# Kernel optimization log

Measured on AMD Instinct MI355X. Metric: run time of the kernel, lower is better.

Reference implementation:

```python
import jax, jax.numpy as jnp
import numpy as np

S, B, D_DEC, D_ALIGN, D_ENC = 1024, 64, 1024, 1024, 1024


def setup_inputs() -> dict:
    key = jax.random.key(0)
    ks = jax.random.split(key, 6)
    scale = 1.0 / np.sqrt(D_DEC)
    return {
        "s_tm1": jax.random.normal(ks[0], (B, D_DEC), jnp.float32),
        "xs_h": jax.random.normal(ks[1], (S, B, D_ENC), jnp.float32),
        "uh": jax.random.normal(ks[2], (S, B, D_ALIGN), jnp.float32),
        "xs_mask": jnp.ones((S, B), jnp.float32),
        "sa_w": jax.random.normal(ks[3], (D_ALIGN, D_DEC), jnp.float32) * scale,
        "sa_b": jnp.zeros((D_ALIGN,), jnp.float32),
        "a1_w": jax.random.normal(ks[4], (1, D_ALIGN), jnp.float32) * scale,
        "a1_b": jnp.zeros((1,), jnp.float32),
    }


def reference(s_tm1, xs_h, uh, xs_mask, sa_w, sa_b, a1_w, a1_b):
    # sa(s_tm1): [B, align]
    sa_s = s_tm1 @ sa_w.T + sa_b
    # broadcast-add over seq dim, tanh, then a1 (align -> 1), squeeze -> [S, B]
    h = jnp.tanh(sa_s[None, :, :] + uh)                  # [S, B, align]
    e = jnp.einsum('sba,a->sb', h, a1_w[0]) + a1_b[0]    # [S, B]
    # masked softmax over dim 0 (seq)
    ex = jnp.exp(e - jnp.max(e, axis=0, keepdims=True))
    ex = ex * xs_mask
    e_ij = ex / jnp.sum(ex, axis=0, keepdims=True)       # [S, B]
    # weighted sum over seq: [B, D_enc]
    attend = jnp.einsum('sb,sbd->bd', e_ij, xs_h)
    return (e_ij, attend)
```

## Files before the change

kernel.cpp:

```cpp
#include <hip/hip_runtime.h>
#include <hip/hip_bf16.h>

#define S_DIM 1024
#define B_DIM 64
#define A_DIM 1024

#define K2_CONST 2.8853900817779268f

#define K_TILE 64
#define KSPLIT 16
#define A_TILE 64
#define SSPLIT 16
#define S_CHUNK 64

__device__ __forceinline__ float fast_exp2(float x) { return __builtin_amdgcn_exp2f(x); }
__device__ __forceinline__ float fast_rcp(float x)  { return __builtin_amdgcn_rcpf(x); }

__global__ __launch_bounds__(256) void gemm_partial_kernel(
    const float* __restrict__ s_tm1,
    const float* __restrict__ sa_w,
    float* __restrict__ part)
{
    __shared__ float sW[K_TILE][68];
    __shared__ float sS[K_TILE][68];
    const int a0 = blockIdx.x * A_TILE;
    const int k0 = blockIdx.y * K_TILE;
    const int t  = threadIdx.x;

    #pragma unroll
    for (int i = 0; i < 4; ++i) {
        int idx = t + 256 * i;
        int row = idx >> 4;
        int c4  = (idx & 15) * 4;
        float4 v = *(const float4*)(sa_w + (size_t)(a0 + row) * 1024 + k0 + c4);
        sW[c4 + 0][row] = v.x; sW[c4 + 1][row] = v.y;
        sW[c4 + 2][row] = v.z; sW[c4 + 3][row] = v.w;
        float4 u = *(const float4*)(s_tm1 + (size_t)row * 1024 + k0 + c4);
        sS[c4 + 0][row] = u.x; sS[c4 + 1][row] = u.y;
        sS[c4 + 2][row] = u.z; sS[c4 + 3][row] = u.w;
    }
    __syncthreads();

    const int ta = (t & 15) * 4;
    const int tb = (t >> 4) * 4;
    float acc[4][4] = {};
    #pragma unroll 8
    for (int k = 0; k < K_TILE; ++k) {
        float4 wa = *(const float4*)&sW[k][ta];
        float4 sb = *(const float4*)&sS[k][tb];
        float wv[4] = {wa.x, wa.y, wa.z, wa.w};
        float sv[4] = {sb.x, sb.y, sb.z, sb.w};
        #pragma unroll
        for (int i = 0; i < 4; ++i)
            #pragma unroll
            for (int j = 0; j < 4; ++j)
                acc[i][j] = fmaf(wv[i], sv[j], acc[i][j]);
    }

    float* outp = part + (size_t)blockIdx.y * (B_DIM * 1024);
    #pragma unroll
    for (int j = 0; j < 4; ++j) {
        float4 v = {acc[0][j], acc[1][j], acc[2][j], acc[3][j]};
        *(float4*)(outp + (size_t)(tb + j) * 1024 + a0 + ta) = v;
    }
}

__global__ __launch_bounds__(256) void gemm_reduce_kernel(
    const float* __restrict__ part, const float* __restrict__ sa_b,
    float* __restrict__ ksa)
{
    int idx = blockIdx.x * 256 + threadIdx.x;
    int a = idx & 1023;
    float s = sa_b[a];
    #pragma unroll
    for (int kz = 0; kz < KSPLIT; ++kz)
        s += part[(size_t)kz * 65536 + idx];
    ksa[idx] = K2_CONST * s;
}

__global__ __launch_bounds__(256) void fused_kernel(
    const float* __restrict__ uh,
    const float* __restrict__ xs_h,
    const float* __restrict__ ksa,
    const float* __restrict__ a1_w,
    const float* __restrict__ xs_mask,
    float* __restrict__ ex_buf,
    float* __restrict__ psum,
    float* __restrict__ part)
{
    const int b    = blockIdx.x;
    const int sz   = blockIdx.y;
    const int s0   = sz * S_CHUNK;
    const int t    = threadIdx.x;
    const int lane = t & 63;
    const int w    = t >> 6;

    __shared__ float s_ex[S_CHUNK];

    const float4* sap = (const float4*)(ksa + (size_t)b * 1024);
    const float4* awp = (const float4*)a1_w;
    float4 sv[4], aw[4];
    #pragma unroll
    for (int j = 0; j < 4; ++j) { sv[j] = sap[lane + 64 * j]; aw[j] = awp[lane + 64 * j]; }

    for (int k = 0; k < 16; ++k) {
        const int i = w + 4 * k;
        const int s = s0 + i;
        const float4* uhp = (const float4*)(uh + ((size_t)s * B_DIM + b) * 1024);
        float mrow = xs_mask[(size_t)s * B_DIM + b];
        float acc = 0.f;
        #pragma unroll
        for (int j = 0; j < 4; ++j) {
            float4 u = uhp[lane + 64 * j];
            float t0 = fast_exp2(fmaf(K2_CONST, u.x, sv[j].x));
            float t1 = fast_exp2(fmaf(K2_CONST, u.y, sv[j].y));
            float t2 = fast_exp2(fmaf(K2_CONST, u.z, sv[j].z));
            float t3 = fast_exp2(fmaf(K2_CONST, u.w, sv[j].w));
            acc = fmaf(aw[j].x, fast_rcp(1.0f + t0), acc);
            acc = fmaf(aw[j].y, fast_rcp(1.0f + t1), acc);
            acc = fmaf(aw[j].z, fast_rcp(1.0f + t2), acc);
            acc = fmaf(aw[j].w, fast_rcp(1.0f + t3), acc);
        }
        #pragma unroll
        for (int off = 32; off; off >>= 1) acc += __shfl_xor(acc, off);
        if (lane == 0) s_ex[i] = fast_exp2(-K2_CONST * acc) * mrow;
    }
    __syncthreads();

    float4 acc4 = {0.f, 0.f, 0.f, 0.f};
    #pragma unroll 8
    for (int i = 0; i < S_CHUNK; ++i) {
        float wgt = s_ex[i];
        float4 x = *(const float4*)(xs_h + (((size_t)(s0 + i) * B_DIM + b) * 1024) + t * 4);
        acc4.x = fmaf(wgt, x.x, acc4.x); acc4.y = fmaf(wgt, x.y, acc4.y);
        acc4.z = fmaf(wgt, x.z, acc4.z); acc4.w = fmaf(wgt, x.w, acc4.w);
    }
    ((float4*)part)[((size_t)sz * B_DIM + b) * 256 + t] = acc4;

    if (t < S_CHUNK)
        ex_buf[(size_t)(s0 + t) * B_DIM + b] = s_ex[t];

    if (w == 0) {
        float v = s_ex[lane];
        #pragma unroll
        for (int off = 32; off; off >>= 1) v += __shfl_xor(v, off);
        if (lane == 0) psum[sz * B_DIM + b] = v;
    }
}

__global__ __launch_bounds__(256) void finalize_kernel(
    const float* __restrict__ ex_buf, const float* __restrict__ part,
    const float* __restrict__ psum,
    float* __restrict__ eij_out, float* __restrict__ att_out)
{
    const int blk = blockIdx.x;
    const int t = threadIdx.x;
    if (blk < 256) {
        int idx = blk * 256 + t;
        int b = idx & 63;
        float ssum = 0.f;
        #pragma unroll
        for (int sz = 0; sz < SSPLIT; ++sz) ssum += psum[sz * B_DIM + b];
        eij_out[idx] = ex_buf[idx] * (1.0f / ssum);
    } else {
        int idx = (blk - 256) * 256 + t;
        int b = idx >> 10;
        float ssum = 0.f;
        #pragma unroll
        for (int sz = 0; sz < SSPLIT; ++sz) ssum += psum[sz * B_DIM + b];
        float acc = 0.f;
        #pragma unroll
        for (int sz = 0; sz < SSPLIT; ++sz) acc += part[(size_t)sz * 65536 + idx];
        att_out[idx] = acc * (1.0f / ssum);
    }
}

extern "C" void kernel_launch(void* const* d_in, const int* in_sizes, int n_in,
                              void* d_out, int out_size, void* d_ws, size_t ws_size,
                              hipStream_t stream) {
    const float* s_tm1   = (const float*)d_in[0];
    const float* xs_h    = (const float*)d_in[1];
    const float* uh      = (const float*)d_in[2];
    const float* xs_mask = (const float*)d_in[3];
    const float* sa_w    = (const float*)d_in[4];
    const float* sa_b    = (const float*)d_in[5];
    const float* a1_w    = (const float*)d_in[6];

    float* eij_out = (float*)d_out;
    float* att_out = (float*)d_out + S_DIM * B_DIM;

    float* part_gemm = (float*)d_ws;
    float* ksa       = part_gemm + (size_t)KSPLIT * B_DIM * 1024;
    float* ex_buf    = ksa + 65536;
    float* part_att  = ex_buf + 65536;
    float* psum      = part_att + (size_t)SSPLIT * B_DIM * 1024;

    gemm_partial_kernel<<<dim3(A_DIM / A_TILE, KSPLIT), 256, 0, stream>>>(s_tm1, sa_w, part_gemm);
    gemm_reduce_kernel<<<65536 / 256, 256, 0, stream>>>(part_gemm, sa_b, ksa);
    fused_kernel<<<dim3(B_DIM, SSPLIT), 256, 0, stream>>>(uh, xs_h, ksa, a1_w, xs_mask,
                                                          ex_buf, psum, part_att);
    finalize_kernel<<<512, 256, 0, stream>>>(ex_buf, part_att, psum, eij_out, att_out);
}
```

Measured before the change: 114.1 us.

## Fuse xs_h weighted sum into score loop per wave with nontemporal uh loads

The attention weighted-sum pass is folded into the per-row score loop: each wave loads its xs_h row alongside the uh row and accumulates ex*xs_h immediately, then the four waves' partials are reduced through shared memory. This removes the barrier-separated second pass over xs_h and lets its loads overlap the tanh/exp work. The mask is preloaded into shared memory, and uh and sa_w use nontemporal loads to avoid polluting cache. In exchange it raises register pressure (xs_h row plus four accumulators) and adds a 16KB shared reduction buffer.

```diff
diff --git a/kernel.cpp b/kernel.cpp
--- a/kernel.cpp
+++ b/kernel.cpp
@@ -13,6 +13,8 @@
 #define SSPLIT 16
 #define S_CHUNK 64
 
+typedef float f4 __attribute__((ext_vector_type(4)));
+
 __device__ __forceinline__ float fast_exp2(float x) { return __builtin_amdgcn_exp2f(x); }
 __device__ __forceinline__ float fast_rcp(float x)  { return __builtin_amdgcn_rcpf(x); }
 
@@ -32,10 +34,10 @@
         int idx = t + 256 * i;
         int row = idx >> 4;
         int c4  = (idx & 15) * 4;
-        float4 v = *(const float4*)(sa_w + (size_t)(a0 + row) * 1024 + k0 + c4);
+        f4 v = __builtin_nontemporal_load((const f4*)(sa_w + (size_t)(a0 + row) * 1024 + k0 + c4));
         sW[c4 + 0][row] = v.x; sW[c4 + 1][row] = v.y;
         sW[c4 + 2][row] = v.z; sW[c4 + 3][row] = v.w;
-        float4 u = *(const float4*)(s_tm1 + (size_t)row * 1024 + k0 + c4);
+        f4 u = *(const f4*)(s_tm1 + (size_t)row * 1024 + k0 + c4);
         sS[c4 + 0][row] = u.x; sS[c4 + 1][row] = u.y;
         sS[c4 + 2][row] = u.z; sS[c4 + 3][row] = u.w;
     }
@@ -46,8 +48,8 @@
     float acc[4][4] = {};
     #pragma unroll 8
     for (int k = 0; k < K_TILE; ++k) {
-        float4 wa = *(const float4*)&sW[k][ta];
-        float4 sb = *(const float4*)&sS[k][tb];
+        f4 wa = *(const f4*)&sW[k][ta];
+        f4 sb = *(const f4*)&sS[k][tb];
         float wv[4] = {wa.x, wa.y, wa.z, wa.w};
         float sv[4] = {sb.x, sb.y, sb.z, sb.w};
         #pragma unroll
@@ -60,8 +62,8 @@
     float* outp = part + (size_t)blockIdx.y * (B_DIM * 1024);
     #pragma unroll
     for (int j = 0; j < 4; ++j) {
-        float4 v = {acc[0][j], acc[1][j], acc[2][j], acc[3][j]};
-        *(float4*)(outp + (size_t)(tb + j) * 1024 + a0 + ta) = v;
+        f4 v = {acc[0][j], acc[1][j], acc[2][j], acc[3][j]};
+        *(f4*)(outp + (size_t)(tb + j) * 1024 + a0 + ta) = v;
     }
 }
 
@@ -96,22 +98,38 @@
     const int w    = t >> 6;
 
     __shared__ float s_ex[S_CHUNK];
-
-    const float4* sap = (const float4*)(ksa + (size_t)b * 1024);
-    const float4* awp = (const float4*)a1_w;
-    float4 sv[4], aw[4];
+    __shared__ float s_mask[S_CHUNK];
+    __shared__ f4 s_red[4][256];
+
+    if (t < S_CHUNK) s_mask[t] = xs_mask[(size_t)(s0 + t) * B_DIM + b];
+
+    const f4* sap = (const f4*)(ksa + (size_t)b * 1024);
+    const f4* awp = (const f4*)a1_w;
+    f4 sv[4], aw[4];
     #pragma unroll
     for (int j = 0; j < 4; ++j) { sv[j] = sap[lane + 64 * j]; aw[j] = awp[lane + 64 * j]; }
 
+    __syncthreads();
+
+    f4 acc4[4];
+    #pragma unroll
+    for (int j = 0; j < 4; ++j) { acc4[j].x = 0.f; acc4[j].y = 0.f; acc4[j].z = 0.f; acc4[j].w = 0.f; }
+
+    #pragma unroll 2
     for (int k = 0; k < 16; ++k) {
         const int i = w + 4 * k;
-        const int s = s0 + i;
-        const float4* uhp = (const float4*)(uh + ((size_t)s * B_DIM + b) * 1024);
-        float mrow = xs_mask[(size_t)s * B_DIM + b];
+        const size_t rowoff = ((size_t)(s0 + i) * B_DIM + b) * 1024;
+        const f4* uhp = (const f4*)(uh + rowoff);
+        const f4* xsp = (const f4*)(xs_h + rowoff);
+
+        f4 xv[4];
+        #pragma unroll
+        for (int j = 0; j < 4; ++j) xv[j] = xsp[lane + 64 * j];
+
         float acc = 0.f;
         #pragma unroll
         for (int j = 0; j < 4; ++j) {
-            float4 u = uhp[lane + 64 * j];
+            f4 u = __builtin_nontemporal_load(&uhp[lane + 64 * j]);
             float t0 = fast_exp2(fmaf(K2_CONST, u.x, sv[j].x));
             float t1 = fast_exp2(fmaf(K2_CONST, u.y, sv[j].y));
             float t2 = fast_exp2(fmaf(K2_CONST, u.z, sv[j].z));
@@ -123,19 +141,30 @@
         }
         #pragma unroll
         for (int off = 32; off; off >>= 1) acc += __shfl_xor(acc, off);
-        if (lane == 0) s_ex[i] = fast_exp2(-K2_CONST * acc) * mrow;
-    }
+
+        float ex = fast_exp2(-K2_CONST * acc) * s_mask[i];
+        if (lane == 0) s_ex[i] = ex;
+
+        #pragma unroll
+        for (int j = 0; j < 4; ++j) {
+            acc4[j].x = fmaf(ex, xv[j].x, acc4[j].x);
+            acc4[j].y = fmaf(ex, xv[j].y, acc4[j].y);
+            acc4[j].z = fmaf(ex, xv[j].z, acc4[j].z);
+            acc4[j].w = fmaf(ex, xv[j].w, acc4[j].w);
+        }
+    }
+
+    #pragma unroll
+    for (int j = 0; j < 4; ++j) s_red[w][lane + 64 * j] = acc4[j];
     __syncthreads();
 
-    float4 acc4 = {0.f, 0.f, 0.f, 0.f};
-    #pragma unroll 8
-    for (int i = 0; i < S_CHUNK; ++i) {
-        float wgt = s_ex[i];
-        float4 x = *(const float4*)(xs_h + (((size_t)(s0 + i) * B_DIM + b) * 1024) + t * 4);
-        acc4.x = fmaf(wgt, x.x, acc4.x); acc4.y = fmaf(wgt, x.y, acc4.y);
-        acc4.z = fmaf(wgt, x.z, acc4.z); acc4.w = fmaf(wgt, x.w, acc4.w);
-    }
-    ((float4*)part)[((size_t)sz * B_DIM + b) * 256 + t] = acc4;
+    f4 r = s_red[0][t];
+    #pragma unroll
+    for (int ww = 1; ww < 4; ++ww) {
+        f4 q = s_red[ww][t];
+        r.x += q.x; r.y += q.y; r.z += q.z; r.w += q.w;
+    }
+    ((f4*)part)[((size_t)sz * B_DIM + b) * 256 + t] = r;
 
     if (t < S_CHUNK)
         ex_buf[(size_t)(s0 + t) * B_DIM + b] = s_ex[t];
```

After: 96.88 us. -15.1%, faster.
